# Optimization experiments

Hardware: AMD Instinct MI355X
Metric: run time of the kernel (lower is better)

Reference implementation:

```python
import jax, jax.numpy as jnp
import numpy as np

N = 100000
NUM_CLASSES = 10
EPS = 1e-16
NEG_SLOPE = 0.2


def gat_conv(x, src, dst, W, a_src, a_dst, bias, heads, out_ch, concat):
    # x: [N, F_in]; src/dst: [E] (message flows src -> dst, PyG convention)
    n = x.shape[0]
    h = (x @ W).reshape(n, heads, out_ch)              # [N, H, C]
    al = jnp.sum(h * a_src, axis=-1)                   # [N, H] source attention term
    ar = jnp.sum(h * a_dst, axis=-1)                   # [N, H] target attention term
    e = jax.nn.leaky_relu(al[src] + ar[dst], NEG_SLOPE)  # [E, H]
    # segment softmax over incoming edges of each dst node
    m = jax.ops.segment_max(e, dst, num_segments=n)    # [N, H]
    ex = jnp.exp(e - m[dst])                           # [E, H]
    denom = jax.ops.segment_sum(ex, dst, num_segments=n)  # [N, H]
    alpha = ex / (denom[dst] + EPS)                    # [E, H]
    msg = h[src] * alpha[..., None]                    # [E, H, C]
    out = jax.ops.segment_sum(msg, dst, num_segments=n)   # [N, H, C]
    out = out.reshape(n, heads * out_ch) if concat else out.mean(axis=1)
    return out + bias


def setup_inputs() -> dict:
    key = jax.random.key(0)
    ks = jax.random.split(key, 10)
    F_in, H1, C1 = 512, 8, 8
    x = jax.random.normal(ks[0], (N, F_in), dtype=jnp.float32)
    edge_index = jax.random.randint(ks[1], (2, 1600000), 0, N, dtype=jnp.int64)
    s = 0.05
    return {
        "x": x,
        "edge_index": edge_index,
        "W1": jax.random.normal(ks[2], (F_in, H1 * C1), dtype=jnp.float32) * s,
        "a_src1": jax.random.normal(ks[3], (H1, C1), dtype=jnp.float32) * s,
        "a_dst1": jax.random.normal(ks[4], (H1, C1), dtype=jnp.float32) * s,
        "b1": jnp.zeros((H1 * C1,), dtype=jnp.float32),
        "W2": jax.random.normal(ks[5], (H1 * C1, NUM_CLASSES), dtype=jnp.float32) * s,
        "a_src2": jax.random.normal(ks[6], (1, NUM_CLASSES), dtype=jnp.float32) * s,
        "a_dst2": jax.random.normal(ks[7], (1, NUM_CLASSES), dtype=jnp.float32) * s,
        "b2": jnp.zeros((NUM_CLASSES,), dtype=jnp.float32),
    }


def reference(x, edge_index, W1, a_src1, a_dst1, b1, W2, a_src2, a_dst2, b2):
    # add self-loops (GATConv default add_self_loops=True)
    loops = jnp.arange(N, dtype=edge_index.dtype)
    src = jnp.concatenate([edge_index[0], loops])
    dst = jnp.concatenate([edge_index[1], loops])
    # eval mode: dropout(p=0.6) is identity
    h = gat_conv(x, src, dst, W1, a_src1, a_dst1, b1, heads=8, out_ch=8, concat=True)
    h = jax.nn.elu(h)
    out = gat_conv(h, src, dst, W2, a_src2, a_dst2, b2, heads=1, out_ch=NUM_CLASSES, concat=True)
    return jax.nn.log_softmax(out, axis=1)
```

## Files before the change

kernel.cpp:

```cpp
#include <hip/hip_runtime.h>
#include <math.h>

#define NN 100000
#define NEDGE 1600000
#define NTOT 1700000
#define FIN 512
#define NH1 8
#define NC1 8
#define F1 64
#define NC2 10
#define SLOPE 0.2f
#define EPSF 1e-16f
#define SCAN_BLK 1024
#define NB ((NN + SCAN_BLK - 1) / SCAN_BLK)

__device__ __forceinline__ float lrelu(float x) { return x > 0.f ? x : SLOPE * x; }
__device__ __forceinline__ float eluf(float x) { return x > 0.f ? x : __expf(x) - 1.f; }

__device__ __forceinline__ int edge_dst(const int* __restrict__ ei, int e) {
    return (e < NEDGE) ? ei[NEDGE + e] : (e - NEDGE);
}
__device__ __forceinline__ int edge_src(const int* __restrict__ ei, int e) {
    return (e < NEDGE) ? ei[e] : (e - NEDGE);
}

#define BM 64
#define BK 32

__global__ __launch_bounds__(256) void k_gemm1(const float* __restrict__ x,
                                               const float* __restrict__ W,
                                               float* __restrict__ h1)
{
    __shared__ float As[BK][BM + 4];
    __shared__ float Bs[BK][F1 + 4];
    const int tid = threadIdx.x;
    const int row0 = blockIdx.x * BM;
    const int ti = tid >> 4, tj = tid & 15;
    float acc[4][4] = {};

    for (int k0 = 0; k0 < FIN; k0 += BK) {
        #pragma unroll
        for (int l = 0; l < 2; ++l) {
            int idx = tid + l * 256;
            int r = idx >> 3, c4 = idx & 7;
            int gr = row0 + r;
            float4 v = make_float4(0.f, 0.f, 0.f, 0.f);
            if (gr < NN) v = *(const float4*)(x + (size_t)gr * FIN + k0 + (c4 << 2));
            As[(c4 << 2) + 0][r] = v.x;
            As[(c4 << 2) + 1][r] = v.y;
            As[(c4 << 2) + 2][r] = v.z;
            As[(c4 << 2) + 3][r] = v.w;
        }
        #pragma unroll
        for (int l = 0; l < 2; ++l) {
            int idx = tid + l * 256;
            int r = idx >> 4, c4 = idx & 15;
            float4 v = *(const float4*)(W + (size_t)(k0 + r) * F1 + (c4 << 2));
            *(float4*)&Bs[r][c4 << 2] = v;
        }
        __syncthreads();
        #pragma unroll
        for (int kk = 0; kk < BK; ++kk) {
            float4 a = *(const float4*)&As[kk][ti << 2];
            float4 b = *(const float4*)&Bs[kk][tj << 2];
            acc[0][0] += a.x * b.x; acc[0][1] += a.x * b.y; acc[0][2] += a.x * b.z; acc[0][3] += a.x * b.w;
            acc[1][0] += a.y * b.x; acc[1][1] += a.y * b.y; acc[1][2] += a.y * b.z; acc[1][3] += a.y * b.w;
            acc[2][0] += a.z * b.x; acc[2][1] += a.z * b.y; acc[2][2] += a.z * b.z; acc[2][3] += a.z * b.w;
            acc[3][0] += a.w * b.x; acc[3][1] += a.w * b.y; acc[3][2] += a.w * b.z; acc[3][3] += a.w * b.w;
        }
        __syncthreads();
    }
    #pragma unroll
    for (int i = 0; i < 4; ++i) {
        int gr = row0 + (ti << 2) + i;
        if (gr < NN) {
            *(float4*)(h1 + (size_t)gr * F1 + (tj << 2)) =
                make_float4(acc[i][0], acc[i][1], acc[i][2], acc[i][3]);
        }
    }
}

__global__ void k_prep1(const float* __restrict__ h1,
                        const float* __restrict__ asrc, const float* __restrict__ adst,
                        float* __restrict__ al, float* __restrict__ ar)
{
    int i = blockIdx.x * blockDim.x + threadIdx.x;
    if (i >= NN * NH1) return;
    int node = i >> 3, hh = i & 7;
    const float* hp = h1 + (size_t)node * F1 + hh * NC1;
    float4 h0 = *(const float4*)hp;
    float4 h4 = *(const float4*)(hp + 4);
    const float* as = asrc + hh * NC1;
    const float* ad = adst + hh * NC1;
    float sa = h0.x * as[0] + h0.y * as[1] + h0.z * as[2] + h0.w * as[3]
             + h4.x * as[4] + h4.y * as[5] + h4.z * as[6] + h4.w * as[7];
    float sd = h0.x * ad[0] + h0.y * ad[1] + h0.z * ad[2] + h0.w * ad[3]
             + h4.x * ad[4] + h4.y * ad[5] + h4.z * ad[6] + h4.w * ad[7];
    al[i] = sa; ar[i] = sd;
}

__global__ void k_zero(int* __restrict__ cnt)
{
    int i = blockIdx.x * blockDim.x + threadIdx.x;
    if (i < NN) cnt[i] = 0;
}

__global__ void k_hist(const int* __restrict__ ei, int* __restrict__ cnt)
{
    int e = blockIdx.x * blockDim.x + threadIdx.x;
    if (e >= NTOT) return;
    atomicAdd(&cnt[edge_dst(ei, e)], 1);
}

__global__ __launch_bounds__(256) void k_scan1(const int* __restrict__ cnt,
                                               int* __restrict__ off,
                                               int* __restrict__ bsum)
{
    __shared__ int s[256];
    int t = threadIdx.x;
    int base = blockIdx.x * SCAN_BLK + t * 4;
    int c0 = (base + 0 < NN) ? cnt[base + 0] : 0;
    int c1 = (base + 1 < NN) ? cnt[base + 1] : 0;
    int c2 = (base + 2 < NN) ? cnt[base + 2] : 0;
    int c3 = (base + 3 < NN) ? cnt[base + 3] : 0;
    int ts = c0 + c1 + c2 + c3;
    s[t] = ts;
    __syncthreads();
    #pragma unroll
    for (int d = 1; d < 256; d <<= 1) {
        int v = (t >= d) ? s[t - d] : 0;
        __syncthreads();
        s[t] += v;
        __syncthreads();
    }
    int run = s[t] - ts;
    if (t == 255) bsum[blockIdx.x] = s[255];
    if (base + 0 < NN) off[base + 0] = run; run += c0;
    if (base + 1 < NN) off[base + 1] = run; run += c1;
    if (base + 2 < NN) off[base + 2] = run; run += c2;
    if (base + 3 < NN) off[base + 3] = run;
}

__global__ void k_scan2(int* __restrict__ bsum, int* __restrict__ off)
{
    if (threadIdx.x == 0 && blockIdx.x == 0) {
        int run = 0;
        for (int b = 0; b < NB; ++b) { int v = bsum[b]; bsum[b] = run; run += v; }
        off[NN] = run;
    }
}

__global__ void k_scan3(int* __restrict__ off, const int* __restrict__ bsum,
                        int* __restrict__ cnt)
{
    int i = blockIdx.x * blockDim.x + threadIdx.x;
    if (i >= NN) return;
    off[i] += bsum[i >> 10];
    cnt[i] = 0;
}

__global__ void k_scatter(const int* __restrict__ ei, const int* __restrict__ off,
                          int* __restrict__ fill, int* __restrict__ esrc)
{
    int e = blockIdx.x * blockDim.x + threadIdx.x;
    if (e >= NTOT) return;
    int d = edge_dst(ei, e);
    int pos = atomicAdd(&fill[d], 1);
    esrc[off[d] + pos] = edge_src(ei, e);
}

__global__ __launch_bounds__(256) void k_agg1csr(const int* __restrict__ off,
                                                 const int* __restrict__ esrc,
                                                 const float* __restrict__ al,
                                                 const float* __restrict__ ar,
                                                 const float* __restrict__ h1,
                                                 const float* __restrict__ b1,
                                                 float* __restrict__ g)
{
    int node = blockIdx.x * 4 + (threadIdx.x >> 6);
    int lane = threadIdx.x & 63;
    int h = lane >> 3;
    int beg = off[node], end = off[node + 1];
    float arn = ar[node * NH1 + h];
    float acc0 = 0.f, acc1 = 0.f, ds0 = 0.f, ds1 = 0.f;
    int i = beg;
    for (; i + 1 < end; i += 2) {
        int s0 = esrc[i], s1 = esrc[i + 1];
        float e0 = __expf(lrelu(al[s0 * NH1 + h] + arn));
        float e1 = __expf(lrelu(al[s1 * NH1 + h] + arn));
        acc0 += h1[(size_t)s0 * F1 + lane] * e0; ds0 += e0;
        acc1 += h1[(size_t)s1 * F1 + lane] * e1; ds1 += e1;
    }
    if (i < end) {
        int s0 = esrc[i];
        float e0 = __expf(lrelu(al[s0 * NH1 + h] + arn));
        acc0 += h1[(size_t)s0 * F1 + lane] * e0; ds0 += e0;
    }
    float v = (acc0 + acc1) / (ds0 + ds1 + EPSF);
    g[(size_t)node * F1 + lane] = eluf(v + b1[lane]);
}

__global__ __launch_bounds__(256) void k_l2prep(
    const float* __restrict__ g, const float* __restrict__ W2,
    const float* __restrict__ asrc2, const float* __restrict__ adst2,
    float* __restrict__ h2, float* __restrict__ al2, float* __restrict__ ar2)
{
    __shared__ float sW[F1 * NC2];
    __shared__ float sas[NC2], sad[NC2];
    int tid = threadIdx.x;
    for (int i = tid; i < F1 * NC2; i += 256) sW[i] = W2[i];
    if (tid < NC2) { sas[tid] = asrc2[tid]; sad[tid] = adst2[tid]; }
    __syncthreads();
    int n = blockIdx.x * 256 + tid;
    if (n >= NN) return;

    const float* row = g + (size_t)n * F1;
    float acc[NC2] = {};
    #pragma unroll
    for (int c = 0; c < F1; c += 4) {
        float4 v = *(const float4*)(row + c);
        #pragma unroll
        for (int o = 0; o < NC2; ++o) {
            acc[o] += v.x * sW[(c + 0) * NC2 + o] + v.y * sW[(c + 1) * NC2 + o]
                    + v.z * sW[(c + 2) * NC2 + o] + v.w * sW[(c + 3) * NC2 + o];
        }
    }
    float sa = 0.f, sd = 0.f;
    #pragma unroll
    for (int o = 0; o < NC2; ++o) { sa += acc[o] * sas[o]; sd += acc[o] * sad[o]; }
    al2[n] = sa; ar2[n] = sd;
    float* h2p = h2 + (size_t)n * NC2;
    #pragma unroll
    for (int o = 0; o < NC2; ++o) h2p[o] = acc[o];
}

__global__ __launch_bounds__(256) void k_agg2csr(const int* __restrict__ off,
                                                 const int* __restrict__ esrc,
                                                 const float* __restrict__ al2,
                                                 const float* __restrict__ ar2,
                                                 const float* __restrict__ h2,
                                                 const float* __restrict__ b2,
                                                 float* __restrict__ out)
{
    int node = blockIdx.x * 16 + (threadIdx.x >> 4);
    int li = threadIdx.x & 15;
    int beg = off[node], end = off[node + 1];
    float arn = ar2[node];
    float acc = 0.f, dsum = 0.f;
    for (int i = beg; i < end; ++i) {
        int s = esrc[i];
        float ev = __expf(lrelu(al2[s] + arn));
        if (li < NC2) acc += h2[(size_t)s * NC2 + li] * ev;
        dsum += ev;
    }
    float z = (li < NC2) ? acc / (dsum + EPSF) + b2[li] : -1e30f;
    float m = z;
    #pragma unroll
    for (int d = 8; d >= 1; d >>= 1) m = fmaxf(m, __shfl_xor(m, d, 16));
    float ex = (li < NC2) ? __expf(z - m) : 0.f;
    float ss = ex;
    #pragma unroll
    for (int d = 8; d >= 1; d >>= 1) ss += __shfl_xor(ss, d, 16);
    float ls = __logf(ss) + m;
    if (li < NC2) out[(size_t)node * NC2 + li] = z - ls;
}

extern "C" void kernel_launch(void* const* d_in, const int* in_sizes, int n_in,
                              void* d_out, int out_size, void* d_ws, size_t ws_size,
                              hipStream_t stream)
{
    const float* x    = (const float*)d_in[0];
    const int*   ei   = (const int*)d_in[1];
    const float* W1   = (const float*)d_in[2];
    const float* as1  = (const float*)d_in[3];
    const float* ad1  = (const float*)d_in[4];
    const float* b1   = (const float*)d_in[5];
    const float* W2   = (const float*)d_in[6];
    const float* as2  = (const float*)d_in[7];
    const float* ad2  = (const float*)d_in[8];
    const float* b2   = (const float*)d_in[9];
    float* out = (float*)d_out;

    float* ws  = (float*)d_ws;
    float* h1  = ws;
    float* al1 = h1 + (size_t)NN * F1;
    float* ar1 = al1 + (size_t)NN * NH1;
    float* g   = ar1 + (size_t)NN * NH1;
    int* cnt   = (int*)(g + (size_t)NN * F1);
    int* off   = cnt + NN;
    int* bsum  = off + NN + 1;
    int* esrc  = bsum + 128;
    float* h2  = h1;
    float* al2 = h1 + (size_t)NN * NC2;
    float* ar2 = al2 + NN;

    k_gemm1<<<(NN + BM - 1) / BM, 256, 0, stream>>>(x, W1, h1);
    k_prep1<<<(NN * NH1 + 255) / 256, 256, 0, stream>>>(h1, as1, ad1, al1, ar1);
    k_zero<<<(NN + 255) / 256, 256, 0, stream>>>(cnt);
    k_hist<<<(NTOT + 255) / 256, 256, 0, stream>>>(ei, cnt);
    k_scan1<<<NB, 256, 0, stream>>>(cnt, off, bsum);
    k_scan2<<<1, 64, 0, stream>>>(bsum, off);
    k_scan3<<<(NN + 255) / 256, 256, 0, stream>>>(off, bsum, cnt);
    k_scatter<<<(NTOT + 255) / 256, 256, 0, stream>>>(ei, off, cnt, esrc);
    k_agg1csr<<<NN / 4, 256, 0, stream>>>(off, esrc, al1, ar1, h1, b1, g);
    k_l2prep<<<(NN + 255) / 256, 256, 0, stream>>>(g, W2, as2, ad2, h2, al2, ar2);
    k_agg2csr<<<NN / 16, 256, 0, stream>>>(off, esrc, al2, ar2, h2, b2, out);
}
```

Before: 676.1 us.

## Fuse attention prep into GEMM, store h1 as bf16, streamline CSR build

The first-layer GEMM now uses a larger 256x64 tile with an 8x8 register micro-tile and computes the per-head source and target attention logits in its epilogue. This removes the separate prep kernel and the re-read of h1 that it needed. h1 is stored as bf16 to halve the gather traffic in the aggregation kernel, at some cost in precision. The CSR build handles self-loops implicitly: counts start at 1 and the loop entry is written first. Edge slots are recorded during the histogram so the scatter needs no second atomic. The single-thread block-sum scan becomes a parallel shared-memory scan.

```diff
diff --git a/kernel.cpp b/kernel.cpp
--- a/kernel.cpp
+++ b/kernel.cpp
@@ -17,30 +17,41 @@
 __device__ __forceinline__ float lrelu(float x) { return x > 0.f ? x : SLOPE * x; }
 __device__ __forceinline__ float eluf(float x) { return x > 0.f ? x : __expf(x) - 1.f; }
 
-__device__ __forceinline__ int edge_dst(const int* __restrict__ ei, int e) {
-    return (e < NEDGE) ? ei[NEDGE + e] : (e - NEDGE);
-}
-__device__ __forceinline__ int edge_src(const int* __restrict__ ei, int e) {
-    return (e < NEDGE) ? ei[e] : (e - NEDGE);
-}
-
-#define BM 64
-#define BK 32
+__device__ __forceinline__ unsigned short f2bf_rne(float f) {
+    unsigned int u = __float_as_uint(f);
+    unsigned int r = (u + 0x7FFFu + ((u >> 16) & 1u)) >> 16;
+    return (unsigned short)r;
+}
+__device__ __forceinline__ float bf2f(unsigned short b) {
+    return __uint_as_float(((unsigned int)b) << 16);
+}
+
+#define GBM 256
+#define GBK 32
+#define AS_STRIDE 260
 
 __global__ __launch_bounds__(256) void k_gemm1(const float* __restrict__ x,
                                                const float* __restrict__ W,
-                                               float* __restrict__ h1)
-{
-    __shared__ float As[BK][BM + 4];
-    __shared__ float Bs[BK][F1 + 4];
+                                               const float* __restrict__ asrc,
+                                               const float* __restrict__ adst,
+                                               unsigned short* __restrict__ h1b,
+                                               float* __restrict__ al,
+                                               float* __restrict__ ar)
+{
+    __shared__ float As[GBK][AS_STRIDE];
+    __shared__ float Bs[GBK][F1];
+    __shared__ float sas[F1], sad[F1];
     const int tid = threadIdx.x;
-    const int row0 = blockIdx.x * BM;
-    const int ti = tid >> 4, tj = tid & 15;
-    float acc[4][4] = {};
-
-    for (int k0 = 0; k0 < FIN; k0 += BK) {
-        #pragma unroll
-        for (int l = 0; l < 2; ++l) {
+    const int row0 = blockIdx.x * GBM;
+    const int ti = tid >> 3;
+    const int tj = tid & 7;
+    const int ti8 = ti << 3, tj8 = tj << 3;
+    if (tid < F1) { sas[tid] = asrc[tid]; sad[tid] = adst[tid]; }
+    float acc[8][8] = {};
+
+    for (int k0 = 0; k0 < FIN; k0 += GBK) {
+        #pragma unroll
+        for (int l = 0; l < 8; ++l) {
             int idx = tid + l * 256;
             int r = idx >> 3, c4 = idx & 7;
             int gr = row0 + r;
@@ -55,61 +66,55 @@
         for (int l = 0; l < 2; ++l) {
             int idx = tid + l * 256;
             int r = idx >> 4, c4 = idx & 15;
-            float4 v = *(const float4*)(W + (size_t)(k0 + r) * F1 + (c4 << 2));
-            *(float4*)&Bs[r][c4 << 2] = v;
-        }
-        __syncthreads();
-        #pragma unroll
-        for (int kk = 0; kk < BK; ++kk) {
-            float4 a = *(const float4*)&As[kk][ti << 2];
-            float4 b = *(const float4*)&Bs[kk][tj << 2];
-            acc[0][0] += a.x * b.x; acc[0][1] += a.x * b.y; acc[0][2] += a.x * b.z; acc[0][3] += a.x * b.w;
-            acc[1][0] += a.y * b.x; acc[1][1] += a.y * b.y; acc[1][2] += a.y * b.z; acc[1][3] += a.y * b.w;
-            acc[2][0] += a.z * b.x; acc[2][1] += a.z * b.y; acc[2][2] += a.z * b.z; acc[2][3] += a.z * b.w;
-            acc[3][0] += a.w * b.x; acc[3][1] += a.w * b.y; acc[3][2] += a.w * b.z; acc[3][3] += a.w * b.w;
-        }
-        __syncthreads();
-    }
-    #pragma unroll
-    for (int i = 0; i < 4; ++i) {
-        int gr = row0 + (ti << 2) + i;
-        if (gr < NN) {
-            *(float4*)(h1 + (size_t)gr * F1 + (tj << 2)) =
-                make_float4(acc[i][0], acc[i][1], acc[i][2], acc[i][3]);
-        }
-    }
-}
-
-__global__ void k_prep1(const float* __restrict__ h1,
-                        const float* __restrict__ asrc, const float* __restrict__ adst,
-                        float* __restrict__ al, float* __restrict__ ar)
+            *(float4*)&Bs[r][c4 << 2] = *(const float4*)(W + (size_t)(k0 + r) * F1 + (c4 << 2));
+        }
+        __syncthreads();
+        #pragma unroll
+        for (int kk = 0; kk < GBK; ++kk) {
+            float4 a0 = *(const float4*)&As[kk][ti8];
+            float4 a1 = *(const float4*)&As[kk][ti8 + 4];
+            float4 b0 = *(const float4*)&Bs[kk][tj8];
+            float4 b1 = *(const float4*)&Bs[kk][tj8 + 4];
+            float a[8] = {a0.x, a0.y, a0.z, a0.w, a1.x, a1.y, a1.z, a1.w};
+            float b[8] = {b0.x, b0.y, b0.z, b0.w, b1.x, b1.y, b1.z, b1.w};
+            #pragma unroll
+            for (int i = 0; i < 8; ++i)
+                #pragma unroll
+                for (int j = 0; j < 8; ++j)
+                    acc[i][j] += a[i] * b[j];
+        }
+        __syncthreads();
+    }
+    #pragma unroll
+    for (int i = 0; i < 8; ++i) {
+        int gr = row0 + ti8 + i;
+        if (gr >= NN) break;
+        float av = 0.f, dv = 0.f;
+        unsigned short u[8];
+        #pragma unroll
+        for (int c = 0; c < 8; ++c) {
+            av += acc[i][c] * sas[tj8 + c];
+            dv += acc[i][c] * sad[tj8 + c];
+            u[c] = f2bf_rne(acc[i][c]);
+        }
+        al[gr * NH1 + tj] = av;
+        ar[gr * NH1 + tj] = dv;
+        *(uint4*)(h1b + (size_t)gr * F1 + tj8) = *(uint4*)u;
+    }
+}
+
+__global__ void k_init1(int* __restrict__ cnt)
 {
     int i = blockIdx.x * blockDim.x + threadIdx.x;
-    if (i >= NN * NH1) return;
-    int node = i >> 3, hh = i & 7;
-    const float* hp = h1 + (size_t)node * F1 + hh * NC1;
-    float4 h0 = *(const float4*)hp;
-    float4 h4 = *(const float4*)(hp + 4);
-    const float* as = asrc + hh * NC1;
-    const float* ad = adst + hh * NC1;
-    float sa = h0.x * as[0] + h0.y * as[1] + h0.z * as[2] + h0.w * as[3]
-             + h4.x * as[4] + h4.y * as[5] + h4.z * as[6] + h4.w * as[7];
-    float sd = h0.x * ad[0] + h0.y * ad[1] + h0.z * ad[2] + h0.w * ad[3]
-             + h4.x * ad[4] + h4.y * ad[5] + h4.z * ad[6] + h4.w * ad[7];
-    al[i] = sa; ar[i] = sd;
-}
-
-__global__ void k_zero(int* __restrict__ cnt)
-{
-    int i = blockIdx.x * blockDim.x + threadIdx.x;
-    if (i < NN) cnt[i] = 0;
-}
-
-__global__ void k_hist(const int* __restrict__ ei, int* __restrict__ cnt)
+    if (i < NN) cnt[i] = 1;
+}
+
+__global__ void k_hist(const int* __restrict__ ei, int* __restrict__ cnt,
+                       int* __restrict__ pos)
 {
     int e = blockIdx.x * blockDim.x + threadIdx.x;
-    if (e >= NTOT) return;
-    atomicAdd(&cnt[edge_dst(ei, e)], 1);
+    if (e >= NEDGE) return;
+    pos[e] = atomicAdd(&cnt[ei[NEDGE + e]], 1);
 }
 
 __global__ __launch_bounds__(256) void k_scan1(const int* __restrict__ cnt,
@@ -143,37 +148,45 @@
 
 __global__ void k_scan2(int* __restrict__ bsum, int* __restrict__ off)
 {
-    if (threadIdx.x == 0 && blockIdx.x == 0) {
-        int run = 0;
-        for (int b = 0; b < NB; ++b) { int v = bsum[b]; bsum[b] = run; run += v; }
-        off[NN] = run;
-    }
+    __shared__ int s[128];
+    int t = threadIdx.x;
+    int v = (t < NB) ? bsum[t] : 0;
+    s[t] = v;
+    __syncthreads();
+    #pragma unroll
+    for (int d = 1; d < 128; d <<= 1) {
+        int w = (t >= d) ? s[t - d] : 0;
+        __syncthreads();
+        s[t] += w;
+        __syncthreads();
+    }
+    if (t < NB) bsum[t] = s[t] - v;
+    if (t == 0) off[NN] = NTOT;
 }
 
 __global__ void k_scan3(int* __restrict__ off, const int* __restrict__ bsum,
-                        int* __restrict__ cnt)
+                        int* __restrict__ esrc)
 {
     int i = blockIdx.x * blockDim.x + threadIdx.x;
     if (i >= NN) return;
-    off[i] += bsum[i >> 10];
-    cnt[i] = 0;
+    int o = off[i] + bsum[i >> 10];
+    off[i] = o;
+    esrc[o] = i;
 }
 
 __global__ void k_scatter(const int* __restrict__ ei, const int* __restrict__ off,
-                          int* __restrict__ fill, int* __restrict__ esrc)
+                          const int* __restrict__ pos, int* __restrict__ esrc)
 {
     int e = blockIdx.x * blockDim.x + threadIdx.x;
-    if (e >= NTOT) return;
-    int d = edge_dst(ei, e);
-    int pos = atomicAdd(&fill[d], 1);
-    esrc[off[d] + pos] = edge_src(ei, e);
+    if (e >= NEDGE) return;
+    esrc[off[ei[NEDGE + e]] + pos[e]] = ei[e];
 }
 
 __global__ __launch_bounds__(256) void k_agg1csr(const int* __restrict__ off,
                                                  const int* __restrict__ esrc,
                                                  const float* __restrict__ al,
                                                  const float* __restrict__ ar,
-                                                 const float* __restrict__ h1,
+                                                 const unsigned short* __restrict__ h1b,
                                                  const float* __restrict__ b1,
                                                  float* __restrict__ g)
 {
@@ -188,13 +201,13 @@
         int s0 = esrc[i], s1 = esrc[i + 1];
         float e0 = __expf(lrelu(al[s0 * NH1 + h] + arn));
         float e1 = __expf(lrelu(al[s1 * NH1 + h] + arn));
-        acc0 += h1[(size_t)s0 * F1 + lane] * e0; ds0 += e0;
-        acc1 += h1[(size_t)s1 * F1 + lane] * e1; ds1 += e1;
+        acc0 += bf2f(h1b[(size_t)s0 * F1 + lane]) * e0; ds0 += e0;
+        acc1 += bf2f(h1b[(size_t)s1 * F1 + lane]) * e1; ds1 += e1;
     }
     if (i < end) {
         int s0 = esrc[i];
         float e0 = __expf(lrelu(al[s0 * NH1 + h] + arn));
-        acc0 += h1[(size_t)s0 * F1 + lane] * e0; ds0 += e0;
+        acc0 += bf2f(h1b[(size_t)s0 * F1 + lane]) * e0; ds0 += e0;
     }
     float v = (acc0 + acc1) / (ds0 + ds1 + EPSF);
     g[(size_t)node * F1 + lane] = eluf(v + b1[lane]);
@@ -281,28 +294,28 @@
     const float* b2   = (const float*)d_in[9];
     float* out = (float*)d_out;
 
-    float* ws  = (float*)d_ws;
-    float* h1  = ws;
-    float* al1 = h1 + (size_t)NN * F1;
+    char* ws = (char*)d_ws;
+    unsigned short* h1b = (unsigned short*)ws;
+    float* al1 = (float*)(ws + (size_t)NN * F1 * 2);
     float* ar1 = al1 + (size_t)NN * NH1;
     float* g   = ar1 + (size_t)NN * NH1;
     int* cnt   = (int*)(g + (size_t)NN * F1);
     int* off   = cnt + NN;
     int* bsum  = off + NN + 1;
     int* esrc  = bsum + 128;
-    float* h2  = h1;
-    float* al2 = h1 + (size_t)NN * NC2;
+    int* pos   = esrc + NTOT;
+    float* h2  = (float*)(pos + NEDGE);
+    float* al2 = h2 + (size_t)NN * NC2;
     float* ar2 = al2 + NN;
 
-    k_gemm1<<<(NN + BM - 1) / BM, 256, 0, stream>>>(x, W1, h1);
-    k_prep1<<<(NN * NH1 + 255) / 256, 256, 0, stream>>>(h1, as1, ad1, al1, ar1);
-    k_zero<<<(NN + 255) / 256, 256, 0, stream>>>(cnt);
-    k_hist<<<(NTOT + 255) / 256, 256, 0, stream>>>(ei, cnt);
+    k_gemm1<<<(NN + GBM - 1) / GBM, 256, 0, stream>>>(x, W1, as1, ad1, h1b, al1, ar1);
+    k_init1<<<(NN + 255) / 256, 256, 0, stream>>>(cnt);
+    k_hist<<<(NEDGE + 255) / 256, 256, 0, stream>>>(ei, cnt, pos);
     k_scan1<<<NB, 256, 0, stream>>>(cnt, off, bsum);
-    k_scan2<<<1, 64, 0, stream>>>(bsum, off);
-    k_scan3<<<(NN + 255) / 256, 256, 0, stream>>>(off, bsum, cnt);
-    k_scatter<<<(NTOT + 255) / 256, 256, 0, stream>>>(ei, off, cnt, esrc);
-    k_agg1csr<<<NN / 4, 256, 0, stream>>>(off, esrc, al1, ar1, h1, b1, g);
+    k_scan2<<<1, 128, 0, stream>>>(bsum, off);
+    k_scan3<<<(NN + 255) / 256, 256, 0, stream>>>(off, bsum, esrc);
+    k_scatter<<<(NEDGE + 255) / 256, 256, 0, stream>>>(ei, off, pos, esrc);
+    k_agg1csr<<<NN / 4, 256, 0, stream>>>(off, esrc, al1, ar1, h1b, b1, g);
     k_l2prep<<<(NN + 255) / 256, 256, 0, stream>>>(g, W2, as2, ad2, h2, al2, ar2);
     k_agg2csr<<<NN / 16, 256, 0, stream>>>(off, esrc, al2, ar2, h2, b2, out);
 }
```

Result: no change. 679.7 us (+0.5%).
